# Performance work log

Measured on AMD Instinct MI355X. Metric: run time of the kernel, lower is better.

The kernel has to match this reference:

```python
import math
import jax, jax.numpy as jnp
import numpy as np

NUM_HEADS = 16
D_MODEL = 1024
B, S = 1, 4096


def setup_inputs() -> dict:
    key = jax.random.key(0)
    ks = jax.random.split(key, 10)
    sc = 1.0 / math.sqrt(D_MODEL)
    # causal mask: 1.0 where masked (strictly upper triangular), 0.0 elsewhere
    causal = jnp.triu(jnp.ones((S, S), dtype=jnp.float32), k=1)
    return {
        "query": jax.random.normal(ks[0], (B, S, D_MODEL), dtype=jnp.float32),
        "mask": jnp.broadcast_to(causal, (B, S, S)),
        "Wq": jax.random.normal(ks[1], (D_MODEL, D_MODEL), dtype=jnp.float32) * sc,
        "bq": jax.random.normal(ks[2], (D_MODEL,), dtype=jnp.float32) * sc,
        "Wk": jax.random.normal(ks[3], (D_MODEL, D_MODEL), dtype=jnp.float32) * sc,
        "bk": jax.random.normal(ks[4], (D_MODEL,), dtype=jnp.float32) * sc,
        "Wv": jax.random.normal(ks[5], (D_MODEL, D_MODEL), dtype=jnp.float32) * sc,
        "bv": jax.random.normal(ks[6], (D_MODEL,), dtype=jnp.float32) * sc,
        "Wo": jax.random.normal(ks[7], (D_MODEL, D_MODEL), dtype=jnp.float32) * sc,
        "bo": jax.random.normal(ks[8], (D_MODEL,), dtype=jnp.float32) * sc,
    }


def _split_heads(x, H, dh):
    # [B,S,D] -> [B,H,S,dh]; head h owns channels [h*dh:(h+1)*dh] (matches the
    # module's transpose->reshape->transpose trick, which equals the contiguous split)
    b, s, _ = x.shape
    return x.reshape(b, s, H, dh).transpose(0, 2, 1, 3)


def reference(query, mask, Wq, bq, Wk, bk, Wv, bv, Wo, bo):
    H = NUM_HEADS
    B_, S_, D = query.shape
    dh = D // H
    q = _split_heads(query @ Wq.T + bq, H, dh)   # [B,H,S,dh]
    k = _split_heads(query @ Wk.T + bk, H, dh)   # self-attention: key = query
    v = _split_heads(query @ Wv.T + bv, H, dh)
    # materialized scores [B,H,S,S]
    scores = jnp.einsum("bhqd,bhkd->bhqk", q, k)
    # mask applied BEFORE the 1/sqrt(d_head) scaling, faithful to the source
    scores = scores + mask[:, None, :, :] * (-1e9)
    attn = jax.nn.softmax(scores / math.sqrt(dh), axis=-1)  # [B,H,S,S]
    out = jnp.einsum("bhqk,bhkd->bhqd", attn, v)            # [B,H,S,dh]
    combined = out.transpose(0, 2, 1, 3).reshape(B_, S_, D)  # [B,S,D]
    return combined @ Wo.T + bo
```

## Files before the change

### kernel.cpp

```cpp
#include <hip/hip_runtime.h>

typedef __bf16 bf16x8 __attribute__((ext_vector_type(8)));
typedef __bf16 bf16x4 __attribute__((ext_vector_type(4)));
typedef float f32x4 __attribute__((ext_vector_type(4)));

typedef const __attribute__((address_space(1))) void* as1_cvp;
typedef __attribute__((address_space(3))) void* as3_vp;
__device__ __forceinline__ void g2l16(const void* g, void* l) {
  __builtin_amdgcn_global_load_lds((as1_cvp)(uintptr_t)g, (as3_vp)(uintptr_t)l, 16, 0, 0);
}

__global__ __launch_bounds__(256) void cast_f32_to_bf16(const float* __restrict__ in,
                                                        __bf16* __restrict__ out, int n4) {
  for (int idx = blockIdx.x * 256 + threadIdx.x; idx < n4; idx += gridDim.x * 256) {
    float4 f = reinterpret_cast<const float4*>(in)[idx];
    bf16x4 t;
    t.x = (__bf16)f.x; t.y = (__bf16)f.y; t.z = (__bf16)f.z; t.w = (__bf16)f.w;
    reinterpret_cast<bf16x4*>(out)[idx] = t;
  }
}

__global__ __launch_bounds__(256) void cast3_f32_to_bf16(const float* __restrict__ w0,
                                                         const float* __restrict__ w1,
                                                         const float* __restrict__ w2,
                                                         __bf16* __restrict__ out, int n4,
                                                         float qs) {
  const float* src = blockIdx.y == 0 ? w0 : (blockIdx.y == 1 ? w1 : w2);
  const float s = blockIdx.y == 0 ? qs : 1.0f;
  __bf16* dst = out + (size_t)blockIdx.y * (size_t)n4 * 4;
  for (int idx = blockIdx.x * 256 + threadIdx.x; idx < n4; idx += gridDim.x * 256) {
    float4 f = reinterpret_cast<const float4*>(src)[idx];
    bf16x4 t;
    t.x = (__bf16)(f.x * s); t.y = (__bf16)(f.y * s);
    t.z = (__bf16)(f.z * s); t.w = (__bf16)(f.w * s);
    reinterpret_cast<bf16x4*>(dst)[idx] = t;
  }
}

template <int BM, typename OUT_T, bool VT_FUSE>
__global__ __launch_bounds__(256) void gemm_bt(const __bf16* __restrict__ A,
                                               const __bf16* __restrict__ B,
                                               const float* __restrict__ b0,
                                               const float* __restrict__ b1,
                                               const float* __restrict__ b2,
                                               OUT_T* __restrict__ C,
                                               __bf16* __restrict__ Vt,
                                               int K, int ldc, float qs) {
  constexpr int MT = BM / 32;
  __shared__ __align__(16) __bf16 Alds[BM][64];
  __shared__ __align__(16) __bf16 Blds[128][64];
  const int tid = threadIdx.x;
  const int wave = tid >> 6, lane = tid & 63;
  const int wm = wave & 1, wn = wave >> 1;
  const int mlane = lane & 15, quad = lane >> 4;
  const int m0 = blockIdx.x * BM, n0 = blockIdx.y * 128;

  f32x4 acc[MT][4] = {};
  constexpr int AN = BM * 8 / 256;

  for (int k0 = 0; k0 < K; k0 += 64) {
#pragma unroll
    for (int j = 0; j < AN; j++) {
      int c = j * 256 + tid;
      g2l16(&A[(size_t)(m0 + (c >> 3)) * K + k0 + (c & 7) * 8], &Alds[0][0] + c * 8);
    }
#pragma unroll
    for (int j = 0; j < 4; j++) {
      int c = j * 256 + tid;
      g2l16(&B[(size_t)(n0 + (c >> 3)) * K + k0 + (c & 7) * 8], &Blds[0][0] + c * 8);
    }
    __syncthreads();
    bf16x8 af[MT][2], bfr[4][2];
#pragma unroll
    for (int mt = 0; mt < MT; mt++)
#pragma unroll
      for (int s = 0; s < 2; s++)
        af[mt][s] = *reinterpret_cast<const bf16x8*>(
            &Alds[wm * (BM / 2) + mt * 16 + mlane][s * 32 + quad * 8]);
#pragma unroll
    for (int nt = 0; nt < 4; nt++)
#pragma unroll
      for (int s = 0; s < 2; s++)
        bfr[nt][s] = *reinterpret_cast<const bf16x8*>(
            &Blds[wn * 64 + nt * 16 + mlane][s * 32 + quad * 8]);
#pragma unroll
    for (int mt = 0; mt < MT; mt++)
#pragma unroll
      for (int nt = 0; nt < 4; nt++)
#pragma unroll
        for (int s = 0; s < 2; s++)
          acc[mt][nt] = __builtin_amdgcn_mfma_f32_16x16x32_bf16(af[mt][s], bfr[nt][s],
                                                                acc[mt][nt], 0, 0, 0);
    __syncthreads();
  }

  const int region = n0 >> 10;
  const float* bp = region == 0 ? b0 : (region == 1 ? b1 : b2);
  const float bs = (region == 0) ? qs : 1.0f;
  float bvs[4];
#pragma unroll
  for (int nt = 0; nt < 4; nt++)
    bvs[nt] = bp[(n0 + wn * 64 + nt * 16 + mlane) & 1023] * bs;

  if (VT_FUSE && region == 2) {
#pragma unroll
    for (int mt = 0; mt < MT; mt++)
#pragma unroll
      for (int nt = 0; nt < 4; nt++) {
        int vcol = ((n0 + wn * 64 + nt * 16 + mlane) & 1023);
        int row0 = m0 + wm * (BM / 2) + mt * 16 + quad * 4;
        bf16x4 t;
#pragma unroll
        for (int r = 0; r < 4; r++) t[r] = (__bf16)(acc[mt][nt][r] + bvs[nt]);
        *reinterpret_cast<bf16x4*>(&Vt[(size_t)vcol * 4096 + row0]) = t;
      }
  } else {
#pragma unroll
    for (int mt = 0; mt < MT; mt++)
#pragma unroll
      for (int nt = 0; nt < 4; nt++) {
        int col = n0 + wn * 64 + nt * 16 + mlane;
#pragma unroll
        for (int r = 0; r < 4; r++) {
          int row = m0 + wm * (BM / 2) + mt * 16 + quad * 4 + r;
          C[(size_t)row * ldc + col] = (OUT_T)(acc[mt][nt][r] + bvs[nt]);
        }
      }
  }
}

__global__ __launch_bounds__(512, 4) void flash_attn(const __bf16* __restrict__ QK,
                                                     const __bf16* __restrict__ Vt,
                                                     __bf16* __restrict__ O, int S) {
  const int LDQ = 2048, D = 1024;
  __shared__ __align__(16) char smem[81920];
  const int tid = threadIdx.x;
  const int wave = tid >> 6, lane = tid & 63;
  const int mlane = lane & 15, quad = lane >> 4;
  const int half = wave >> 2, rw = wave & 3;
  const int b = blockIdx.x, h = blockIdx.y;

  __bf16* Pw = (__bf16*)(smem + 65536) + wave * 1024;

  for (int pass = 0; pass < 2; ++pass) {
    const int qb = pass ? b : (63 - b);
    const int qbase = qb * 64 + rw * 16;

    bf16x8 qf[2];
#pragma unroll
    for (int s = 0; s < 2; s++)
      qf[s] = *reinterpret_cast<const bf16x8*>(
          &QK[(size_t)(qbase + mlane) * LDQ + h * 64 + s * 32 + quad * 8]);

    f32x4 o[4] = {};
    float lrow[4] = {0.f, 0.f, 0.f, 0.f};

    const int nkb = qb / 2 + 1;

    auto STAGE = [&](int t, int buf) {
      char* kd = smem + buf * 16384;
      char* vd = smem + 32768 + buf * 16384;
#pragma unroll
      for (int j = 0; j < 2; j++) {
        int c = j * 512 + tid;
        int r = c >> 3, sl = c & 7;
        g2l16(&QK[(size_t)(t * 128 + r) * LDQ + 1024 + h * 64 + ((sl ^ (r & 7)) * 8)],
              kd + c * 16);
      }
#pragma unroll
      for (int j = 0; j < 2; j++) {
        int c = j * 512 + tid;
        int r = c >> 4, sl = c & 15;
        g2l16(&Vt[(size_t)(h * 64 + r) * S + t * 128 + ((sl ^ (r & 15)) * 8)],
              vd + c * 16);
      }
    };

    STAGE(0, 0);
    __syncthreads();

    for (int kb = 0; kb < nkb; ++kb) {
      const int buf = kb & 1;
      __bf16(*Klds)[64] = (__bf16(*)[64])(smem + buf * 16384);
      __bf16(*Vlds)[128] = (__bf16(*)[128])(smem + 32768 + buf * 16384);

      if (kb + 1 < nkb) STAGE(kb + 1, buf ^ 1);

      f32x4 sc[4];
#pragma unroll
      for (int nt = 0; nt < 4; nt++) {
        f32x4 a = {};
#pragma unroll
        for (int s = 0; s < 2; s++) {
          bf16x8 bk = *reinterpret_cast<const bf16x8*>(
              &Klds[half * 64 + nt * 16 + mlane][((4 * s + quad) ^ (mlane & 7)) * 8]);
          a = __builtin_amdgcn_mfma_f32_16x16x32_bf16(qf[s], bk, a, 0, 0, 0);
        }
        sc[nt] = a;
      }

      const bool maskTile = (kb == nkb - 1);
#pragma unroll
      for (int r = 0; r < 4; r++) {
        if (maskTile) {
          const int qg = qbase + quad * 4 + r;
#pragma unroll
          for (int nt = 0; nt < 4; nt++) {
            int kg = kb * 128 + half * 64 + nt * 16 + mlane;
            if (kg > qg) sc[nt][r] = -INFINITY;
          }
        }
        float ls = 0.f;
#pragma unroll
        for (int nt = 0; nt < 4; nt++) {
          float p = __builtin_amdgcn_exp2f(sc[nt][r]);
          sc[nt][r] = p;
          ls += p;
        }
        lrow[r] += ls;
        const int prow = quad * 4 + r, rx = prow & 7;
#pragma unroll
        for (int nt = 0; nt < 4; nt++) {
          int pcol = nt * 16 + mlane;
          Pw[prow * 64 + (((pcol >> 3) ^ rx) * 8) + (pcol & 7)] = (__bf16)sc[nt][r];
        }
      }

#pragma unroll
      for (int s = 0; s < 2; s++) {
        bf16x8 pf = *reinterpret_cast<const bf16x8*>(
            &Pw[mlane * 64 + (((4 * s + quad) ^ (mlane & 7)) * 8)]);
#pragma unroll
        for (int nt = 0; nt < 4; nt++) {
          bf16x8 vf = *reinterpret_cast<const bf16x8*>(
              &Vlds[nt * 16 + mlane][((half * 8 + s * 4 + quad) ^ mlane) * 8]);
          o[nt] = __builtin_amdgcn_mfma_f32_16x16x32_bf16(pf, vf, o[nt], 0, 0, 0);
        }
      }
      __syncthreads();
    }

    float* osc = (float*)smem;
    float* lsc = (float*)(smem + 17408);
    if (half == 1) {
      const int ob = (rw * 64 + lane) * 17, lb = (rw * 64 + lane) * 5;
#pragma unroll
      for (int nt = 0; nt < 4; nt++)
#pragma unroll
        for (int r = 0; r < 4; r++) osc[ob + nt * 4 + r] = o[nt][r];
#pragma unroll
      for (int r = 0; r < 4; r++) lsc[lb + r] = lrow[r];
    }
    __syncthreads();
    if (half == 0) {
      const int ob = (rw * 64 + lane) * 17, lb = (rw * 64 + lane) * 5;
#pragma unroll
      for (int nt = 0; nt < 4; nt++)
#pragma unroll
        for (int r = 0; r < 4; r++) o[nt][r] += osc[ob + nt * 4 + r];
#pragma unroll
      for (int r = 0; r < 4; r++) {
        float l = lrow[r] + lsc[lb + r];
#pragma unroll
        for (int off = 1; off < 16; off <<= 1) l += __shfl_xor(l, off, 64);
        float inv = 1.0f / l;
        int row = qbase + quad * 4 + r;
#pragma unroll
        for (int nt = 0; nt < 4; nt++)
          O[(size_t)row * D + h * 64 + nt * 16 + mlane] = (__bf16)(o[nt][r] * inv);
      }
    }
    __syncthreads();
  }
}

extern "C" void kernel_launch(void* const* d_in, const int* in_sizes, int n_in,
                              void* d_out, int out_size, void* d_ws, size_t ws_size,
                              hipStream_t stream) {
  const float* query = (const float*)d_in[0];
  const float* Wq = (const float*)d_in[2];
  const float* bq = (const float*)d_in[3];
  const float* Wk = (const float*)d_in[4];
  const float* bk = (const float*)d_in[5];
  const float* Wv = (const float*)d_in[6];
  const float* bv = (const float*)d_in[7];
  const float* Wo = (const float*)d_in[8];
  const float* bo = (const float*)d_in[9];
  float* out = (float*)d_out;

  const int S = 4096, D = 1024;
  const float SCL = 0.125f * 1.44269504088896340736f;
  char* ws = (char*)d_ws;
  __bf16* Xb   = (__bf16*)(ws);
  __bf16* Cb   = (__bf16*)(ws);
  __bf16* Wqkv = (__bf16*)(ws + (8u << 20));
  __bf16* Wob  = (__bf16*)(ws + (14u << 20));
  __bf16* QKb  = (__bf16*)(ws + (16u << 20));
  __bf16* Vt   = (__bf16*)(ws + (32u << 20));

  cast_f32_to_bf16<<<1024, 256, 0, stream>>>(query, Xb, S * D / 4);
  cast3_f32_to_bf16<<<dim3(256, 3), 256, 0, stream>>>(Wq, Wk, Wv, Wqkv, D * D / 4, SCL);
  cast_f32_to_bf16<<<256, 256, 0, stream>>>(Wo, Wob, D * D / 4);

  gemm_bt<128, __bf16, true><<<dim3(S / 128, 3 * D / 128), 256, 0, stream>>>(
      Xb, Wqkv, bq, bk, bv, QKb, Vt, D, 2048, SCL);

  flash_attn<<<dim3(32, 16), 512, 0, stream>>>(QKb, Vt, Cb, S);

  gemm_bt<64, float, false><<<dim3(S / 64, D / 128), 256, 0, stream>>>(
      Cb, Wob, bo, bo, bo, out, nullptr, D, D, 1.0f);
}
```

Before: 263.1 us.

## Merge cast kernels and transpose score MFMA so P is stored vectorized

The three cast launches are merged into one 2D-grid kernel covering the query and all four weight matrices, which removes two launch overheads. In flash attention the QK^T MFMA operands are swapped, so each lane holds four consecutive keys for a single query row. That lets P be written to LDS as one bf16x4 store per tile instead of scalar stores. The row-sum then reduces with two shuffles instead of per-row 16-lane reductions. The masking and LDS swizzle indexing are rewritten to match the transposed layout.

```diff
diff --git a/kernel.cpp b/kernel.cpp
--- a/kernel.cpp
+++ b/kernel.cpp
@@ -10,24 +10,30 @@
   __builtin_amdgcn_global_load_lds((as1_cvp)(uintptr_t)g, (as3_vp)(uintptr_t)l, 16, 0, 0);
 }
 
-__global__ __launch_bounds__(256) void cast_f32_to_bf16(const float* __restrict__ in,
-                                                        __bf16* __restrict__ out, int n4) {
-  for (int idx = blockIdx.x * 256 + threadIdx.x; idx < n4; idx += gridDim.x * 256) {
-    float4 f = reinterpret_cast<const float4*>(in)[idx];
-    bf16x4 t;
-    t.x = (__bf16)f.x; t.y = (__bf16)f.y; t.z = (__bf16)f.z; t.w = (__bf16)f.w;
-    reinterpret_cast<bf16x4*>(out)[idx] = t;
-  }
-}
-
-__global__ __launch_bounds__(256) void cast3_f32_to_bf16(const float* __restrict__ w0,
-                                                         const float* __restrict__ w1,
-                                                         const float* __restrict__ w2,
-                                                         __bf16* __restrict__ out, int n4,
-                                                         float qs) {
-  const float* src = blockIdx.y == 0 ? w0 : (blockIdx.y == 1 ? w1 : w2);
-  const float s = blockIdx.y == 0 ? qs : 1.0f;
-  __bf16* dst = out + (size_t)blockIdx.y * (size_t)n4 * 4;
+__global__ __launch_bounds__(256) void cast_all(const float* __restrict__ q,
+                                                const float* __restrict__ wq,
+                                                const float* __restrict__ wk,
+                                                const float* __restrict__ wv,
+                                                const float* __restrict__ wo,
+                                                __bf16* __restrict__ xb,
+                                                __bf16* __restrict__ wqkv,
+                                                __bf16* __restrict__ wob, float qs) {
+  const int y = blockIdx.y;
+  const float* src;
+  __bf16* dst;
+  int n4;
+  float s = 1.0f;
+  if (y == 0) {
+    src = q; dst = xb; n4 = 1048576;
+  } else if (y == 1) {
+    src = wq; dst = wqkv; n4 = 262144; s = qs;
+  } else if (y == 2) {
+    src = wk; dst = wqkv + 1048576; n4 = 262144;
+  } else if (y == 3) {
+    src = wv; dst = wqkv + 2097152; n4 = 262144;
+  } else {
+    src = wo; dst = wob; n4 = 262144;
+  }
   for (int idx = blockIdx.x * 256 + threadIdx.x; idx < n4; idx += gridDim.x * 256) {
     float4 f = reinterpret_cast<const float4*>(src)[idx];
     bf16x4 t;
@@ -139,12 +145,14 @@
   const int mlane = lane & 15, quad = lane >> 4;
   const int half = wave >> 2, rw = wave & 3;
   const int b = blockIdx.x, h = blockIdx.y;
-
-  __bf16* Pw = (__bf16*)(smem + 65536) + wave * 1024;
+  const int m7 = mlane & 7;
+
+  char* Pw = smem + 65536 + wave * 2048;
 
   for (int pass = 0; pass < 2; ++pass) {
     const int qb = pass ? b : (63 - b);
     const int qbase = qb * 64 + rw * 16;
+    const int qg = qbase + mlane;
 
     bf16x8 qf[2];
 #pragma unroll
@@ -153,7 +161,7 @@
           &QK[(size_t)(qbase + mlane) * LDQ + h * 64 + s * 32 + quad * 8]);
 
     f32x4 o[4] = {};
-    float lrow[4] = {0.f, 0.f, 0.f, 0.f};
+    float lsum = 0.f;
 
     const int nkb = qb / 2 + 1;
 
@@ -193,43 +201,39 @@
 #pragma unroll
         for (int s = 0; s < 2; s++) {
           bf16x8 bk = *reinterpret_cast<const bf16x8*>(
-              &Klds[half * 64 + nt * 16 + mlane][((4 * s + quad) ^ (mlane & 7)) * 8]);
-          a = __builtin_amdgcn_mfma_f32_16x16x32_bf16(qf[s], bk, a, 0, 0, 0);
+              &Klds[half * 64 + nt * 16 + mlane][((4 * s + quad) ^ m7) * 8]);
+          a = __builtin_amdgcn_mfma_f32_16x16x32_bf16(bk, qf[s], a, 0, 0, 0);
         }
         sc[nt] = a;
       }
 
       const bool maskTile = (kb == nkb - 1);
 #pragma unroll
-      for (int r = 0; r < 4; r++) {
+      for (int nt = 0; nt < 4; nt++) {
         if (maskTile) {
-          const int qg = qbase + quad * 4 + r;
-#pragma unroll
-          for (int nt = 0; nt < 4; nt++) {
-            int kg = kb * 128 + half * 64 + nt * 16 + mlane;
-            if (kg > qg) sc[nt][r] = -INFINITY;
-          }
-        }
-        float ls = 0.f;
-#pragma unroll
-        for (int nt = 0; nt < 4; nt++) {
+          const int kg0 = kb * 128 + half * 64 + nt * 16 + quad * 4;
+#pragma unroll
+          for (int r = 0; r < 4; r++)
+            if (kg0 + r > qg) sc[nt][r] = -INFINITY;
+        }
+#pragma unroll
+        for (int r = 0; r < 4; r++) {
           float p = __builtin_amdgcn_exp2f(sc[nt][r]);
           sc[nt][r] = p;
-          ls += p;
-        }
-        lrow[r] += ls;
-        const int prow = quad * 4 + r, rx = prow & 7;
-#pragma unroll
-        for (int nt = 0; nt < 4; nt++) {
-          int pcol = nt * 16 + mlane;
-          Pw[prow * 64 + (((pcol >> 3) ^ rx) * 8) + (pcol & 7)] = (__bf16)sc[nt][r];
-        }
+          lsum += p;
+        }
+        bf16x4 t;
+#pragma unroll
+        for (int r = 0; r < 4; r++) t[r] = (__bf16)sc[nt][r];
+        const int s8 = nt * 4 + quad;
+        *reinterpret_cast<bf16x4*>(Pw + mlane * 128 + (((s8 >> 1) ^ m7) * 16) +
+                                   ((s8 & 1) * 8)) = t;
       }
 
 #pragma unroll
       for (int s = 0; s < 2; s++) {
         bf16x8 pf = *reinterpret_cast<const bf16x8*>(
-            &Pw[mlane * 64 + (((4 * s + quad) ^ (mlane & 7)) * 8)]);
+            Pw + mlane * 128 + (((4 * s + quad) ^ m7) * 16));
 #pragma unroll
         for (int nt = 0; nt < 4; nt++) {
           bf16x8 vf = *reinterpret_cast<const bf16x8*>(
@@ -240,29 +244,29 @@
       __syncthreads();
     }
 
+    lsum += __shfl_xor(lsum, 16, 64);
+    lsum += __shfl_xor(lsum, 32, 64);
+
     float* osc = (float*)smem;
     float* lsc = (float*)(smem + 17408);
+    if (lane < 16) lsc[half * 64 + rw * 16 + lane] = lsum;
     if (half == 1) {
-      const int ob = (rw * 64 + lane) * 17, lb = (rw * 64 + lane) * 5;
+      const int ob = (rw * 64 + lane) * 17;
 #pragma unroll
       for (int nt = 0; nt < 4; nt++)
 #pragma unroll
         for (int r = 0; r < 4; r++) osc[ob + nt * 4 + r] = o[nt][r];
-#pragma unroll
-      for (int r = 0; r < 4; r++) lsc[lb + r] = lrow[r];
     }
     __syncthreads();
     if (half == 0) {
-      const int ob = (rw * 64 + lane) * 17, lb = (rw * 64 + lane) * 5;
+      const int ob = (rw * 64 + lane) * 17;
 #pragma unroll
       for (int nt = 0; nt < 4; nt++)
 #pragma unroll
         for (int r = 0; r < 4; r++) o[nt][r] += osc[ob + nt * 4 + r];
 #pragma unroll
       for (int r = 0; r < 4; r++) {
-        float l = lrow[r] + lsc[lb + r];
-#pragma unroll
-        for (int off = 1; off < 16; off <<= 1) l += __shfl_xor(l, off, 64);
+        float l = lsc[rw * 16 + quad * 4 + r] + lsc[64 + rw * 16 + quad * 4 + r];
         float inv = 1.0f / l;
         int row = qbase + quad * 4 + r;
 #pragma unroll
@@ -298,9 +302,7 @@
   __bf16* QKb  = (__bf16*)(ws + (16u << 20));
   __bf16* Vt   = (__bf16*)(ws + (32u << 20));
 
-  cast_f32_to_bf16<<<1024, 256, 0, stream>>>(query, Xb, S * D / 4);
-  cast3_f32_to_bf16<<<dim3(256, 3), 256, 0, stream>>>(Wq, Wk, Wv, Wqkv, D * D / 4, SCL);
-  cast_f32_to_bf16<<<256, 256, 0, stream>>>(Wo, Wob, D * D / 4);
+  cast_all<<<dim3(512, 5), 256, 0, stream>>>(query, Wq, Wk, Wv, Wo, Xb, Wqkv, Wob, SCL);
 
   gemm_bt<128, __bf16, true><<<dim3(S / 128, 3 * D / 128), 256, 0, stream>>>(
       Xb, Wqkv, bq, bk, bv, QKb, Vt, D, 2048, SCL);
```

Measured after the change: 252.3 us. 4.1% less time.
